# Kernel optimization log

Measured on AMD Instinct MI355X. Metric: run time of the kernel, lower is better.

## Reference

```python
import jax, jax.numpy as jnp
import numpy as np

C = 300      # caption feature dim (word2vec)
OQK = 75     # in_dim // k = 300 // 4 -> query/key channels
H = 128      # adapt_img_hidden (base_proj dim)
LAT = 1024   # image latent size
EPS = 1e-5   # BatchNorm eps


def setup_inputs() -> dict:
    key = jax.random.key(0)
    ks = jax.random.split(key, 16)
    r = lambda i, shape, s=0.05: jax.random.normal(ks[i], shape, dtype=jnp.float32) * s
    return dict(
        img_embed=jax.random.normal(ks[0], (128, 36, LAT), dtype=jnp.float32),
        cap_embed=jax.random.normal(ks[1], (64, 32, C), dtype=jnp.float32),
        # adapt_img: Linear(1024, 128)
        adapt_W=r(2, (H, LAT)), adapt_b=jnp.zeros((H,), jnp.float32),
        # query ProjConv1d: kernel Linear(H, OQK*C), bias Linear(H, OQK), BatchNorm1d(OQK)
        qk_W=r(3, (OQK * C, H)), qk_b=r(4, (OQK * C,)),
        qb_W=r(5, (OQK, H)), qb_b=jnp.zeros((OQK,), jnp.float32),
        q_bn_s=jnp.ones((OQK,), jnp.float32), q_bn_b=jnp.zeros((OQK,), jnp.float32),
        # key ProjConv1d
        kk_W=r(6, (OQK * C, H)), kk_b=r(7, (OQK * C,)),
        kb_W=r(8, (OQK, H)), kb_b=jnp.zeros((OQK,), jnp.float32),
        k_bn_s=jnp.ones((OQK,), jnp.float32), k_bn_b=jnp.zeros((OQK,), jnp.float32),
        # value ProjConv1d: kernel Linear(H, C*C), bias Linear(H, C), BatchNorm1d(C)
        vk_W=r(9, (C * C, H)), vk_b=r(10, (C * C,)),
        vb_W=r(11, (C, H)), vb_b=jnp.zeros((C,), jnp.float32),
        v_bn_s=jnp.ones((C,), jnp.float32), v_bn_b=jnp.zeros((C,), jnp.float32),
        gamma=jnp.float32(0.5),  # residual attention gate (torch inits to 0; 0.5 exercises the path)
        # sim_proj MLP: 300 -> 512 -> 64 -> 1 with BatchNorm+ReLU (dropout = identity at eval)
        W1=r(12, (512, C)), b1=jnp.zeros((512,), jnp.float32),
        bn1_s=jnp.ones((512,), jnp.float32), bn1_b=jnp.zeros((512,), jnp.float32),
        W2=r(13, (64, 512)), b2=jnp.zeros((64,), jnp.float32),
        bn2_s=jnp.ones((64,), jnp.float32), bn2_b=jnp.zeros((64,), jnp.float32),
        W3=r(14, (1, 64)), b3=jnp.zeros((1,), jnp.float32),
    )


def _bn_kernel(kern, s, b):
    # torch: BatchNorm1d(out)(kernel.permute(1,0,2)) with kernel (out, in, ks=1)
    # -> per out-channel stats over the `in` axis (train-mode batch stats)
    mu = kern.mean(axis=1, keepdims=True)
    var = kern.var(axis=1, keepdims=True)
    return (kern - mu) / jnp.sqrt(var + EPS) * s[:, None] + b[:, None]


def _bn_batch(x, s, b):
    # BatchNorm1d over batch axis of (N, C) activations (train-mode stats)
    mu = x.mean(axis=0, keepdims=True)
    var = x.var(axis=0, keepdims=True)
    return (x - mu) / jnp.sqrt(var + EPS) * s + b


def reference(img_embed, cap_embed, adapt_W, adapt_b,
              qk_W, qk_b, qb_W, qb_b, q_bn_s, q_bn_b,
              kk_W, kk_b, kb_W, kb_b, k_bn_s, k_bn_b,
              vk_W, vk_b, vb_W, vb_b, v_bn_s, v_bn_b,
              gamma, W1, b1, bn1_s, bn1_b, W2, b2, bn2_s, bn2_b, W3, b3):
    cap = cap_embed.transpose(0, 2, 1)                      # (Bc, C, T)
    img_mean = img_embed.transpose(0, 2, 1).mean(-1)        # (Bi, LAT): mean over 36 regions
    base = img_mean @ adapt_W.T + adapt_b                   # (Bi, H)

    def per_image(bp):
        # hypernet-generated 1x1 conv kernels, batchnorm-normalized
        Kq = _bn_kernel((qk_W @ bp + qk_b).reshape(OQK, C), q_bn_s, q_bn_b)
        Kk = _bn_kernel((kk_W @ bp + kk_b).reshape(OQK, C), k_bn_s, k_bn_b)
        Kv = _bn_kernel((vk_W @ bp + vk_b).reshape(C, C), v_bn_s, v_bn_b)
        bq = qb_W @ bp + qb_b
        bk = kb_W @ bp + kb_b
        bv = vb_W @ bp + vb_b
        q = jnp.einsum('oc,nct->not', Kq, cap) + bq[:, None]    # (Bc, OQK, T)
        k = jnp.einsum('oc,nct->not', Kk, cap) + bk[:, None]    # (Bc, OQK, T)
        v = jnp.einsum('oc,nct->not', Kv, cap) + bv[:, None]    # (Bc, C, T)
        attn = jax.nn.softmax(jnp.einsum('not,nos->nts', q, k), axis=-1)  # (Bc, T, T)
        sa = jnp.einsum('ncs,nts->nct', v, attn)                # out = V @ attn^T
        x = (gamma * sa + cap).max(-1)                          # (Bc, C): max-pool over tokens
        h = jax.nn.relu(_bn_batch(x @ W1.T + b1, bn1_s, bn1_b))
        h = jax.nn.relu(_bn_batch(h @ W2.T + b2, bn2_s, bn2_b))
        return (h @ W3.T + b3)[:, 0]                            # (Bc,)

    return jax.vmap(per_image)(base)                            # (Bi, Bc)
```

## Files before the change

kernel.cpp:

```cpp
#include <hip/hip_runtime.h>
#include <math.h>

#define EPSB 1e-5f

static const long OFS_BASE  = 0;
static const long OFS_BALL  = 16384;
static const long OFS_MEAN  = 81920;
static const long OFS_CAPB  = 212992;
static const long OFS_RAWP  = 868352;
static const long OFS_X     = 15286272;
static const long OFS_H2    = 17743872;
static const long OFS_H1    = OFS_RAWP;

using bf16x8 = __attribute__((ext_vector_type(8))) __bf16;
using f32x4  = __attribute__((ext_vector_type(4))) float;
#define MFMA16(a, b, c) __builtin_amdgcn_mfma_f32_16x16x32_bf16(a, b, c, 0, 0, 0)

__device__ inline ushort f2bf(float f) {
  const unsigned u = __float_as_uint(f);
  return (ushort)((u + 0x7FFFu + ((u >> 16) & 1u)) >> 16);
}
__device__ inline float bf2f(ushort h) { return __uint_as_float(((unsigned)h) << 16); }

__global__ void k_mean(const float* __restrict__ img, float* __restrict__ mean) {
  const int idx = blockIdx.x * 256 + threadIdx.x;
  const int i = idx >> 10, l = idx & 1023;
  const float* p = img + (size_t)i * 36 * 1024 + l;
  float s = 0.f;
#pragma unroll
  for (int r = 0; r < 36; ++r) s += p[r * 1024];
  mean[idx] = s * (1.0f / 36.0f);
}

__global__ void k_base(const float* __restrict__ mean, const float* __restrict__ W,
                       const float* __restrict__ b, float* __restrict__ base) {
  __shared__ float m_s[1024];
  const int i = blockIdx.x, tid = threadIdx.x;
  for (int k = 0; k < 8; ++k) m_s[tid + 128 * k] = mean[i * 1024 + tid + 128 * k];
  __syncthreads();
  float acc = b[tid];
  const float* wr = W + (size_t)tid * 1024;
#pragma unroll 4
  for (int l = 0; l < 1024; ++l) acc = fmaf(m_s[l], wr[l], acc);
  base[i * 128 + tid] = acc;
}

__global__ void k_bias(const float* __restrict__ qbW, const float* __restrict__ qbb,
                       const float* __restrict__ kbW, const float* __restrict__ kbb,
                       const float* __restrict__ vbW, const float* __restrict__ vbb,
                       const float* __restrict__ base, float* __restrict__ ball) {
  __shared__ float bs[128];
  const int i = blockIdx.y, tid = threadIdx.x;
  if (tid < 128) bs[tid] = base[i * 128 + tid];
  __syncthreads();
  const int o = blockIdx.x * 256 + tid;
  if (o >= 512) return;
  const float* Wr = nullptr;
  float bb = 0.0f;
  if (o < 75)                   { Wr = qbW + (size_t)o * 128;         bb = qbb[o]; }
  else if (o >= 96 && o < 171)  { Wr = kbW + (size_t)(o - 96) * 128;  bb = kbb[o - 96]; }
  else if (o >= 192 && o < 492) { Wr = vbW + (size_t)(o - 192) * 128; bb = vbb[o - 192]; }
  float acc = 0.0f;
  if (Wr) {
#pragma unroll 4
    for (int h = 0; h < 128; ++h) acc = fmaf(Wr[h], bs[h], acc);
    acc += bb;
  }
  ball[i * 512 + o] = acc;
}

__global__ void __launch_bounds__(256) k_capp(const float* __restrict__ cap,
                                              ushort* __restrict__ capP) {
  __shared__ float ct[32 * 301];
  const int n = blockIdx.x, tid = threadIdx.x;
  const float* capn = cap + (size_t)n * 9600;
  {
    const int r = tid >> 3, c8 = tid & 7;
    for (int m = 0; m < 38; ++m) {
      const int c = c8 + 8 * m;
      if (c < 300) ct[r * 301 + c] = capn[r * 300 + c];
    }
  }
  __syncthreads();
  ushort* dst = capP + (size_t)n * 20480;
  for (int u = 0; u < 10; ++u) {
    const int ul = tid + 256 * u;
    const int unit = ul >> 6, lane = ul & 63;
    const int nt = unit / 20, rem = unit % 20;
    const int ks = rem >> 1, pl = rem & 1;
    const int kg = lane >> 4, lr = lane & 15;
    const int t = nt * 16 + lr;
    ushort o8[8];
#pragma unroll
    for (int e = 0; e < 8; ++e) {
      const int c = 32 * ks + 8 * kg + e;
      const float val = (c < 300) ? ct[t * 301 + c] : 0.f;
      const ushort hi = f2bf(val);
      o8[e] = pl ? f2bf(val - bf2f(hi)) : hi;
    }
    uint4 pk;
    pk.x = (uint)o8[0] | ((uint)o8[1] << 16);
    pk.y = (uint)o8[2] | ((uint)o8[3] << 16);
    pk.z = (uint)o8[4] | ((uint)o8[5] << 16);
    pk.w = (uint)o8[6] | ((uint)o8[7] << 16);
    *reinterpret_cast<uint4*>(dst + unit * 512 + lane * 8) = pk;
  }
}

__global__ void __launch_bounds__(256) k_hyp3(
    const float* __restrict__ qkW, const float* __restrict__ qkb,
    const float* __restrict__ kkW, const float* __restrict__ kkb,
    const float* __restrict__ vkW, const float* __restrict__ vkb,
    const float* __restrict__ qs, const float* __restrict__ qb,
    const float* __restrict__ ks_, const float* __restrict__ kb_,
    const float* __restrict__ vs, const float* __restrict__ vb,
    const float* __restrict__ base, ushort* __restrict__ kall) {
  __shared__ float smem[19504];
  __shared__ float scl[64], shf[64];
  const int g = blockIdx.x, half = blockIdx.y, tid = threadIdx.x;
  const int i0g = half * 64;
  const int ot = g >> 4, lr = g & 15;
  const bool isV = (g >= 192);

  const float* Wb = nullptr;
  const float* bvec = nullptr;
  float bns = 0.f, bnb = 0.f;
  if (g < 75)                    { Wb = qkW + (size_t)g * 38400;          bvec = qkb + g * 300;          bns = qs[g];        bnb = qb[g]; }
  else if (g >= 96 && g < 171)   { Wb = kkW + (size_t)(g - 96) * 38400;   bvec = kkb + (g - 96) * 300;   bns = ks_[g - 96];  bnb = kb_[g - 96]; }
  else if (g >= 192 && g < 492)  { Wb = vkW + (size_t)(g - 192) * 38400;  bvec = vkb + (g - 192) * 300;  bns = vs[g - 192];  bnb = vb[g - 192]; }

  if (!Wb) {
    const uint4 z = make_uint4(0, 0, 0, 0);
    if (!isV) {
      for (int m = 0; m < 20; ++m) {
        const int idx = tid + 256 * m;
        const int ii = idx & 63, zz = idx >> 6;
        const int kg2 = zz & 3, pl = (zz >> 2) & 1, ks2 = zz >> 3;
        const size_t off = (size_t)(i0g + ii) * 225280 +
                           (size_t)(ot * 20 + ks2 * 2 + pl) * 512 + (kg2 * 16 + lr) * 8;
        *reinterpret_cast<uint4*>(kall + off) = z;
      }
    } else {
      for (int m = 0; m < 10; ++m) {
        const int idx = tid + 256 * m;
        const int ii = idx & 63, zz = idx >> 6;
        const int kg2 = zz & 3, ks2 = zz >> 2;
        const size_t off = (size_t)(i0g + ii) * 225280 +
                           (size_t)(240 + (ot - 12) * 10 + ks2) * 512 + (kg2 * 16 + lr) * 8;
        *reinterpret_cast<uint4*>(kall + off) = z;
      }
    }
    return;
  }

  for (int m = 0; m < 32; ++m) {
    const int idx = tid + 256 * m;
    const int ii = idx >> 7, h = idx & 127;
    smem[h * 68 + ii] = base[(size_t)(i0g + ii) * 128 + h];
  }

  const int cg = tid >> 2, ig = tid & 3;
  const int c0 = cg * 5, i0 = ig * 16;
  float acc[5][16];
#pragma unroll
  for (int cc = 0; cc < 5; ++cc)
#pragma unroll
    for (int ii = 0; ii < 16; ++ii) acc[cc][ii] = 0.f;
  float* Ws = smem + 8704;
  for (int hc = 0; hc < 4; ++hc) {
    __syncthreads();
    for (int m = 0; m < 10; ++m) {
      const int u = tid + 256 * m;
      if (u < 2400) {
        const int c = u >> 3, h4 = (u & 7) * 4;
        const float4 wv4 = *reinterpret_cast<const float4*>(Wb + (size_t)c * 128 + hc * 32 + h4);
        *reinterpret_cast<float4*>(&Ws[c * 36 + h4]) = wv4;
      }
    }
    __syncthreads();
#pragma unroll 4
    for (int hh = 0; hh < 32; ++hh) {
      const int hg = hc * 32 + hh;
      float bvf[16];
#pragma unroll
      for (int u2 = 0; u2 < 4; ++u2) {
        const float4 b4 = *reinterpret_cast<const float4*>(&smem[hg * 68 + i0 + u2 * 4]);
        bvf[u2 * 4 + 0] = b4.x; bvf[u2 * 4 + 1] = b4.y;
        bvf[u2 * 4 + 2] = b4.z; bvf[u2 * 4 + 3] = b4.w;
      }
#pragma unroll
      for (int cc = 0; cc < 5; ++cc) {
        const float wv = Ws[(c0 + cc) * 36 + hh];
#pragma unroll
        for (int ii = 0; ii < 16; ++ii) acc[cc][ii] = fmaf(wv, bvf[ii], acc[cc][ii]);
      }
    }
  }
  __syncthreads();
#pragma unroll
  for (int cc = 0; cc < 5; ++cc) {
    const int c = c0 + cc;
    if (c < 300) {
      const float bv = bvec[c];
#pragma unroll
      for (int ii = 0; ii < 16; ++ii) smem[c * 64 + i0 + ii] = acc[cc][ii] + bv;
    }
  }
  __syncthreads();
  {
    const int si = tid >> 2, p = tid & 3;
    float s1 = 0.f, s2 = 0.f;
    for (int c = p; c < 300; c += 4) {
      const float x = smem[c * 64 + si];
      s1 += x;
      s2 += x * x;
    }
    s1 += __shfl_xor(s1, 1); s2 += __shfl_xor(s2, 1);
    s1 += __shfl_xor(s1, 2); s2 += __shfl_xor(s2, 2);
    const float mu = s1 * (1.0f / 300.0f);
    const float var = s2 * (1.0f / 300.0f) - mu * mu;
    const float scale = bns / sqrtf(var + EPSB);
    if (p == 0) { scl[si] = scale; shf[si] = bnb - mu * scale; }
  }
  __syncthreads();
  if (!isV) {
    for (int m = 0; m < 20; ++m) {
      const int idx = tid + 256 * m;
      const int ii = idx & 63, zz = idx >> 6;
      const int kg2 = zz & 3, pl = (zz >> 2) & 1, ks2 = zz >> 3;
      const float sc = scl[ii], sh = shf[ii];
      ushort o8[8];
#pragma unroll
      for (int e = 0; e < 8; ++e) {
        const int c = ks2 * 32 + kg2 * 8 + e;
        float val = 0.f;
        if (c < 300) val = fmaf(smem[c * 64 + ii], sc, sh);
        const ushort hi = f2bf(val);
        o8[e] = pl ? f2bf(val - bf2f(hi)) : hi;
      }
      uint4 pk;
      pk.x = (uint)o8[0] | ((uint)o8[1] << 16);
      pk.y = (uint)o8[2] | ((uint)o8[3] << 16);
      pk.z = (uint)o8[4] | ((uint)o8[5] << 16);
      pk.w = (uint)o8[6] | ((uint)o8[7] << 16);
      const size_t off = (size_t)(i0g + ii) * 225280 +
                         (size_t)(ot * 20 + ks2 * 2 + pl) * 512 + (kg2 * 16 + lr) * 8;
      *reinterpret_cast<uint4*>(kall + off) = pk;
    }
  } else {
    for (int m = 0; m < 10; ++m) {
      const int idx = tid + 256 * m;
      const int ii = idx & 63, zz = idx >> 6;
      const int kg2 = zz & 3, ks2 = zz >> 2;
      const float sc = scl[ii], sh = shf[ii];
      ushort o8[8];
#pragma unroll
      for (int e = 0; e < 8; ++e) {
        const int c = ks2 * 32 + kg2 * 8 + e;
        float val = 0.f;
        if (c < 300) val = fmaf(smem[c * 64 + ii], sc, sh);
        o8[e] = f2bf(val);
      }
      uint4 pk;
      pk.x = (uint)o8[0] | ((uint)o8[1] << 16);
      pk.y = (uint)o8[2] | ((uint)o8[3] << 16);
      pk.z = (uint)o8[4] | ((uint)o8[5] << 16);
      pk.w = (uint)o8[6] | ((uint)o8[7] << 16);
      const size_t off = (size_t)(i0g + ii) * 225280 +
                         (size_t)(240 + (ot - 12) * 10 + ks2) * 512 + (kg2 * 16 + lr) * 8;
      *reinterpret_cast<uint4*>(kall + off) = pk;
    }
  }
}

__global__ void __launch_bounds__(256, 4) k_attn10(
    const float* __restrict__ cap, const ushort* __restrict__ kall,
    const ushort* __restrict__ capP, const float* __restrict__ ball,
    const float* __restrict__ gptr, float* __restrict__ x_all) {
  __shared__ ushort qkp[24 * 512];
  __shared__ float sc_s[32 * 36];
  __shared__ ushort at_p[2 * 2 * 64 * 8];
  const int bid = blockIdx.x;
  const int xcd = bid & 7, q = bid >> 3;
  const int i = xcd * 16 + (q >> 6), n = q & 63;
  const int tid = threadIdx.x;
  const int lane = tid & 63, w = tid >> 6;
  const int lrow = lane & 15, kg = lane >> 4;
  const float gamma = gptr[0];
  const ushort* kpL = kall + (size_t)i * 225280 + lane * 8;
  const ushort* cpL = capP + (size_t)n * 20480 + lane * 8;
  const float* bal = ball + i * 512;

  {
    f32x4 acc[3][2];
#pragma unroll
    for (int a = 0; a < 3; ++a)
#pragma unroll
      for (int b2 = 0; b2 < 2; ++b2) acc[a][b2] = (f32x4){0.f, 0.f, 0.f, 0.f};
    bf16x8 AhA[3], AlA[3], AhB[3], AlB[3];
#pragma unroll
    for (int mt = 0; mt < 3; ++mt) {
      const ushort* p = kpL + (size_t)((w * 3 + mt) * 20) * 512;
      AhA[mt] = *reinterpret_cast<const bf16x8*>(p);
      AlA[mt] = *reinterpret_cast<const bf16x8*>(p + 512);
    }
#pragma unroll
    for (int kp = 0; kp < 5; ++kp) {
      {
        const int ks = 2 * kp;
        bf16x8 Bh[2], Bl[2];
#pragma unroll
        for (int nt = 0; nt < 2; ++nt) {
          const ushort* p = cpL + (size_t)(nt * 20 + ks * 2) * 512;
          Bh[nt] = *reinterpret_cast<const bf16x8*>(p);
          Bl[nt] = *reinterpret_cast<const bf16x8*>(p + 512);
        }
#pragma unroll
        for (int mt = 0; mt < 3; ++mt) {
          const ushort* p = kpL + (size_t)((w * 3 + mt) * 20 + (ks + 1) * 2) * 512;
          AhB[mt] = *reinterpret_cast<const bf16x8*>(p);
          AlB[mt] = *reinterpret_cast<const bf16x8*>(p + 512);
        }
#pragma unroll
        for (int mt = 0; mt < 3; ++mt)
#pragma unroll
          for (int nt = 0; nt < 2; ++nt) {
            acc[mt][nt] = MFMA16(AhA[mt], Bh[nt], acc[mt][nt]);
            acc[mt][nt] = MFMA16(AhA[mt], Bl[nt], acc[mt][nt]);
            acc[mt][nt] = MFMA16(AlA[mt], Bh[nt], acc[mt][nt]);
          }
      }
      {
        const int ks = 2 * kp + 1;
        bf16x8 Bh[2], Bl[2];
#pragma unroll
        for (int nt = 0; nt < 2; ++nt) {
          const ushort* p = cpL + (size_t)(nt * 20 + ks * 2) * 512;
          Bh[nt] = *reinterpret_cast<const bf16x8*>(p);
          Bl[nt] = *reinterpret_cast<const bf16x8*>(p + 512);
        }
        if (kp < 4) {
#pragma unroll
          for (int mt = 0; mt < 3; ++mt) {
            const ushort* p = kpL + (size_t)((w * 3 + mt) * 20 + (ks + 1) * 2) * 512;
            AhA[mt] = *reinterpret_cast<const bf16x8*>(p);
            AlA[mt] = *reinterpret_cast<const bf16x8*>(p + 512);
          }
        }
#pragma unroll
        for (int mt = 0; mt < 3; ++mt)
#pragma unroll
          for (int nt = 0; nt < 2; ++nt) {
            acc[mt][nt] = MFMA16(AhB[mt], Bh[nt], acc[mt][nt]);
            acc[mt][nt] = MFMA16(AhB[mt], Bl[nt], acc[mt][nt]);
            acc[mt][nt] = MFMA16(AlB[mt], Bh[nt], acc[mt][nt]);
          }
      }
    }
#pragma unroll
    for (int mt = 0; mt < 3; ++mt)
#pragma unroll
      for (int nt = 0; nt < 2; ++nt)
#pragma unroll
        for (int r = 0; r < 4; ++r) {
          const int og = w * 48 + mt * 16 + kg * 4 + r;
          const float val = acc[mt][nt][r] + bal[og];
          const ushort hi = f2bf(val);
          const ushort lo = f2bf(val - bf2f(hi));
          const int os = (w < 2) ? og : og - 96;
          const int ub = ((w < 2) ? 0 : 12) + nt * 6 + (os >> 5) * 2;
          const int lp = ((os & 31) >> 3) * 16 + lrow;
          const int e = os & 7;
          qkp[(ub + 0) * 512 + lp * 8 + e] = hi;
          qkp[(ub + 1) * 512 + lp * 8 + e] = lo;
        }
  }
  __syncthreads();

  {
    const int tt = w >> 1, st = w & 1;
    bf16x8 Aq[3][2], Bk[3][2];
#pragma unroll
    for (int k3 = 0; k3 < 3; ++k3)
#pragma unroll
      for (int pl = 0; pl < 2; ++pl) {
        Aq[k3][pl] = *reinterpret_cast<const bf16x8*>(&qkp[(tt * 6 + k3 * 2 + pl) * 512 + lane * 8]);
        Bk[k3][pl] = *reinterpret_cast<const bf16x8*>(&qkp[(12 + st * 6 + k3 * 2 + pl) * 512 + lane * 8]);
      }
    f32x4 D = (f32x4){0.f, 0.f, 0.f, 0.f};
#pragma unroll
    for (int k3 = 0; k3 < 3; ++k3) {
      D = MFMA16(Aq[k3][0], Bk[k3][0], D);
      D = MFMA16(Aq[k3][0], Bk[k3][1], D);
      D = MFMA16(Aq[k3][1], Bk[k3][0], D);
      D = MFMA16(Aq[k3][1], Bk[k3][1], D);
    }
#pragma unroll
    for (int r = 0; r < 4; ++r)
      sc_s[(tt * 16 + kg * 4 + r) * 36 + st * 16 + lrow] = D[r];
  }
  __syncthreads();

  {
    const int sg = tid & 7, tq = tid >> 3;
    const int s0 = sg * 4;
    const float4 sv = *reinterpret_cast<const float4*>(&sc_s[tq * 36 + s0]);
    float sc[4] = {sv.x, sv.y, sv.z, sv.w};
    float m = fmaxf(fmaxf(sc[0], sc[1]), fmaxf(sc[2], sc[3]));
    m = fmaxf(m, __shfl_xor(m, 1));
    m = fmaxf(m, __shfl_xor(m, 2));
    m = fmaxf(m, __shfl_xor(m, 4));
    float ev[4], ssum = 0.f;
#pragma unroll
    for (int u = 0; u < 4; ++u) { ev[u] = expf(sc[u] - m); ssum += ev[u]; }
    ssum += __shfl_xor(ssum, 1);
    ssum += __shfl_xor(ssum, 2);
    ssum += __shfl_xor(ssum, 4);
    const float inv = 1.0f / ssum;
    const int tt = tq >> 4, lrp = tq & 15, kgp = sg >> 1, eb = (sg & 1) * 4;
    ushort h4[4], l4[4];
#pragma unroll
    for (int u = 0; u < 4; ++u) {
      const float val = ev[u] * inv;
      const ushort hi = f2bf(val);
      h4[u] = hi;
      l4[u] = f2bf(val - bf2f(hi));
    }
    uint2 ph, pl2;
    ph.x = (uint)h4[0] | ((uint)h4[1] << 16);
    ph.y = (uint)h4[2] | ((uint)h4[3] << 16);
    pl2.x = (uint)l4[0] | ((uint)l4[1] << 16);
    pl2.y = (uint)l4[2] | ((uint)l4[3] << 16);
    *reinterpret_cast<uint2*>(&at_p[((tt * 2 + 0) * 64 + kgp * 16 + lrp) * 8 + eb]) = ph;
    *reinterpret_cast<uint2*>(&at_p[((tt * 2 + 1) * 64 + kgp * 16 + lrp) * 8 + eb]) = pl2;
  }
  __syncthreads();

  ushort* vt = qkp;
#pragma unroll
  for (int ch = 0; ch < 2; ++ch) {
    const int TB = 12 + ch * 12;
    const int RB = TB * 16;
    const int nmt = ch ? 2 : 3;
    f32x4 vacc[3][2];
#pragma unroll
    for (int a = 0; a < 3; ++a)
#pragma unroll
      for (int b2 = 0; b2 < 2; ++b2) vacc[a][b2] = (f32x4){0.f, 0.f, 0.f, 0.f};
    bf16x8 AvA[3], AvB[3];
    for (int mi = 0; mi < nmt; ++mi)
      AvA[mi] = *reinterpret_cast<const bf16x8*>(
          kpL + (size_t)(240 + (TB - 12 + w + mi * 4) * 10) * 512);
#pragma unroll
    for (int kp = 0; kp < 5; ++kp) {
      {
        const int ks = 2 * kp;
        bf16x8 Bh[2];
#pragma unroll
        for (int nt = 0; nt < 2; ++nt)
          Bh[nt] = *reinterpret_cast<const bf16x8*>(cpL + (size_t)(nt * 20 + ks * 2) * 512);
        for (int mi = 0; mi < nmt; ++mi)
          AvB[mi] = *reinterpret_cast<const bf16x8*>(
              kpL + (size_t)(240 + (TB - 12 + w + mi * 4) * 10 + ks + 1) * 512);
        for (int mi = 0; mi < nmt; ++mi)
#pragma unroll
          for (int nt = 0; nt < 2; ++nt)
            vacc[mi][nt] = MFMA16(AvA[mi], Bh[nt], vacc[mi][nt]);
      }
      {
        const int ks = 2 * kp + 1;
        bf16x8 Bh[2];
#pragma unroll
        for (int nt = 0; nt < 2; ++nt)
          Bh[nt] = *reinterpret_cast<const bf16x8*>(cpL + (size_t)(nt * 20 + ks * 2) * 512);
        if (kp < 4) {
          for (int mi = 0; mi < nmt; ++mi)
            AvA[mi] = *reinterpret_cast<const bf16x8*>(
                kpL + (size_t)(240 + (TB - 12 + w + mi * 4) * 10 + ks + 1) * 512);
        }
        for (int mi = 0; mi < nmt; ++mi)
#pragma unroll
          for (int nt = 0; nt < 2; ++nt)
            vacc[mi][nt] = MFMA16(AvB[mi], Bh[nt], vacc[mi][nt]);
      }
    }
    if (ch) __syncthreads();
    for (int mi = 0; mi < nmt; ++mi) {
      const int tile = w + mi * 4;
#pragma unroll
      for (int nt = 0; nt < 2; ++nt) {
        const int kgp = nt * 2 + (lrow >> 3), ee = lrow & 7;
#pragma unroll
        for (int r = 0; r < 4; ++r) {
          const int vl = tile * 16 + kg * 4 + r;
          const float val = vacc[mi][nt][r] + bal[RB + vl];
          const ushort hi = f2bf(val);
          vt[((tile * 2 + 0) * 64 + kgp * 16 + kg * 4 + r) * 8 + ee] = hi;
          vt[((tile * 2 + 1) * 64 + kgp * 16 + kg * 4 + r) * 8 + ee] = f2bf(val - bf2f(hi));
        }
      }
    }
    __syncthreads();
    {
      bf16x8 ah[2], al[2];
#pragma unroll
      for (int tt = 0; tt < 2; ++tt) {
        ah[tt] = *reinterpret_cast<const bf16x8*>(&at_p[((tt * 2 + 0) * 64 + lane) * 8]);
        al[tt] = *reinterpret_cast<const bf16x8*>(&at_p[((tt * 2 + 1) * 64 + lane) * 8]);
      }
      const int npw = ch ? 2 : 3;
      for (int j = 0; j < npw; ++j) {
        const int ct = w * npw + j;
        const int c0 = ch * 192 + ct * 16 + (lane >> 4) * 4;
        const bf16x8 vh  = *reinterpret_cast<const bf16x8*>(&vt[((ct * 2 + 0) * 64 + lane) * 8]);
        const bf16x8 vl8 = *reinterpret_cast<const bf16x8*>(&vt[((ct * 2 + 1) * 64 + lane) * 8]);
        f32x4 a0 = (f32x4){0.f, 0.f, 0.f, 0.f}, a1 = (f32x4){0.f, 0.f, 0.f, 0.f};
        a0 = MFMA16(vh, ah[0], a0);
        a0 = MFMA16(vh, al[0], a0);
        a0 = MFMA16(vl8, ah[0], a0);
        a1 = MFMA16(vh, ah[1], a1);
        a1 = MFMA16(vh, al[1], a1);
        a1 = MFMA16(vl8, ah[1], a1);
        if (c0 < 300) {
          const int t0 = lane & 15;
          const float4 c4a = *reinterpret_cast<const float4*>(&cap[(size_t)n * 9600 + t0 * 300 + c0]);
          const float4 c4b = *reinterpret_cast<const float4*>(&cap[(size_t)n * 9600 + (t0 + 16) * 300 + c0]);
          float mx[4];
          mx[0] = fmaxf(fmaf(gamma, a0[0], c4a.x), fmaf(gamma, a1[0], c4b.x));
          mx[1] = fmaxf(fmaf(gamma, a0[1], c4a.y), fmaf(gamma, a1[1], c4b.y));
          mx[2] = fmaxf(fmaf(gamma, a0[2], c4a.z), fmaf(gamma, a1[2], c4b.z));
          mx[3] = fmaxf(fmaf(gamma, a0[3], c4a.w), fmaf(gamma, a1[3], c4b.w));
#pragma unroll
          for (int mmask = 1; mmask < 16; mmask <<= 1)
#pragma unroll
            for (int r = 0; r < 4; ++r) mx[r] = fmaxf(mx[r], __shfl_xor(mx[r], mmask));
          if ((lane & 15) == 0)
            *reinterpret_cast<float4*>(&x_all[((size_t)i * 64 + n) * 300 + c0]) =
                make_float4(mx[0], mx[1], mx[2], mx[3]);
        }
      }
    }
  }
}

__global__ void __launch_bounds__(256, 4) k_h1b(
    const float* __restrict__ x_all, const float* __restrict__ W1,
    const float* __restrict__ b1, const float* __restrict__ bn1s,
    const float* __restrict__ bn1b, float* __restrict__ h1) {
  __shared__ float xt[32 * 68];
  __shared__ float wt[32 * 132];
  __shared__ float sc1[128], sh1[128];
  const int ec = blockIdx.x, i = blockIdx.y, tid = threadIdx.x;
  const int e0c = ec * 128;
  const int eg = tid & 15, ng = tid >> 4;
  const int e0 = eg * 8, n0 = ng * 4;
  float acc[4][8] = {};
  for (int cb = 0; cb < 10; ++cb) {
    const int c0 = cb * 32;
    __syncthreads();
    for (int k = 0; k < 8; ++k) {
      const int idx = tid + 256 * k;
      const int nn = idx >> 5, cl = idx & 31;
      const int c = c0 + cl;
      xt[cl * 68 + nn] = (c < 300) ? x_all[((size_t)i * 64 + nn) * 300 + c] : 0.0f;
    }
    for (int k = 0; k < 16; ++k) {
      const int idx = tid + 256 * k;
      const int ee = idx >> 5, cl = idx & 31;
      const int c = c0 + cl;
      wt[cl * 132 + ee] = (c < 300) ? W1[(size_t)(e0c + ee) * 300 + c] : 0.0f;
    }
    __syncthreads();
#pragma unroll 4
    for (int cl = 0; cl < 32; ++cl) {
      const float4 xv = *reinterpret_cast<const float4*>(&xt[cl * 68 + n0]);
      const float4 wa = *reinterpret_cast<const float4*>(&wt[cl * 132 + e0]);
      const float4 wb = *reinterpret_cast<const float4*>(&wt[cl * 132 + e0 + 4]);
      const float xv4[4] = {xv.x, xv.y, xv.z, xv.w};
      const float wv8[8] = {wa.x, wa.y, wa.z, wa.w, wb.x, wb.y, wb.z, wb.w};
#pragma unroll
      for (int u = 0; u < 4; ++u)
#pragma unroll
        for (int v = 0; v < 8; ++v) acc[u][v] = fmaf(xv4[u], wv8[v], acc[u][v]);
    }
  }
  float b1v[8];
#pragma unroll
  for (int v = 0; v < 8; ++v) b1v[v] = b1[e0c + e0 + v];
  float val[4][8];
#pragma unroll
  for (int u = 0; u < 4; ++u)
#pragma unroll
    for (int v = 0; v < 8; ++v) val[u][v] = acc[u][v] + b1v[v];
  __syncthreads();
  float* ps1 = xt;
  float* ps2 = wt;
#pragma unroll
  for (int v = 0; v < 8; ++v) {
    float su = 0.f, sq = 0.f;
#pragma unroll
    for (int u = 0; u < 4; ++u) { su += val[u][v]; sq += val[u][v] * val[u][v]; }
    ps1[ng * 132 + e0 + v] = su;
    ps2[ng * 132 + e0 + v] = sq;
  }
  __syncthreads();
  if (tid < 128) {
    const int e = tid;
    float s1 = 0.f, s2 = 0.f;
#pragma unroll 4
    for (int gq = 0; gq < 16; ++gq) { s1 += ps1[gq * 132 + e]; s2 += ps2[gq * 132 + e]; }
    const float mu = s1 * (1.0f / 64.0f);
    const float var = s2 * (1.0f / 64.0f) - mu * mu;
    const float scale = bn1s[e0c + e] / sqrtf(var + EPSB);
    sc1[e] = scale;
    sh1[e] = bn1b[e0c + e] - mu * scale;
  }
  __syncthreads();
#pragma unroll
  for (int u = 0; u < 4; ++u) {
    float o8[8];
#pragma unroll
    for (int v = 0; v < 8; ++v)
      o8[v] = fmaxf(fmaf(val[u][v], sc1[e0 + v], sh1[e0 + v]), 0.0f);
    float* dst = h1 + ((size_t)i * 64 + n0 + u) * 512 + e0c + e0;
    *reinterpret_cast<float4*>(dst) = make_float4(o8[0], o8[1], o8[2], o8[3]);
    *reinterpret_cast<float4*>(dst + 4) = make_float4(o8[4], o8[5], o8[6], o8[7]);
  }
}

__global__ void __launch_bounds__(256) k_h2(
    const float* __restrict__ h1, const float* __restrict__ W2,
    const float* __restrict__ b2, float* __restrict__ h2buf) {
  __shared__ float h1s[32 * 517];
  const int jn = blockIdx.x, i = blockIdx.y, tid = threadIdx.x;
  const int bn = jn * 32;
  for (int m = 0; m < 64; ++m) {
    const int idx = tid + 256 * m;
    h1s[(idx >> 9) * 517 + (idx & 511)] = h1[((size_t)i * 64 + bn) * 512 + idx];
  }
  __syncthreads();
  const int dg = tid & 15, ng2 = tid >> 4;
  const int d0 = dg * 4, n0 = ng2 * 2;
  float a0[4] = {}, a1[4] = {};
#pragma unroll 4
  for (int e = 0; e < 512; ++e) {
    const float h0 = h1s[n0 * 517 + e];
    const float h1v = h1s[(n0 + 1) * 517 + e];
#pragma unroll
    for (int v = 0; v < 4; ++v) {
      const float wv = W2[(size_t)(d0 + v) * 512 + e];
      a0[v] = fmaf(h0, wv, a0[v]);
      a1[v] = fmaf(h1v, wv, a1[v]);
    }
  }
  const float4 bb = *reinterpret_cast<const float4*>(&b2[d0]);
  float* dst0 = h2buf + ((size_t)i * 64 + bn + n0) * 64 + d0;
  *reinterpret_cast<float4*>(dst0) = make_float4(a0[0] + bb.x, a0[1] + bb.y, a0[2] + bb.z, a0[3] + bb.w);
  *reinterpret_cast<float4*>(dst0 + 64) = make_float4(a1[0] + bb.x, a1[1] + bb.y, a1[2] + bb.z, a1[3] + bb.w);
}

__global__ void __launch_bounds__(256) k_out(
    const float* __restrict__ h2buf, const float* __restrict__ bn2s,
    const float* __restrict__ bn2b, const float* __restrict__ W3,
    const float* __restrict__ b3, float* __restrict__ out) {
  __shared__ float h2s[64 * 65];
  const int i = blockIdx.x, tid = threadIdx.x;
  for (int m = 0; m < 16; ++m) {
    const int idx = tid + 256 * m;
    h2s[(idx >> 6) * 65 + (idx & 63)] = h2buf[(size_t)i * 4096 + idx];
  }
  __syncthreads();
  if (tid < 64) {
    const int d = tid;
    float s1 = 0.f, s2 = 0.f;
    for (int nn = 0; nn < 64; ++nn) {
      const float v = h2s[nn * 65 + d];
      s1 += v;
      s2 += v * v;
    }
    const float mu = s1 * (1.0f / 64.0f);
    const float var = s2 * (1.0f / 64.0f) - mu * mu;
    const float scale = bn2s[d] / sqrtf(var + EPSB);
    const float shift = bn2b[d] - mu * scale;
    for (int nn = 0; nn < 64; ++nn)
      h2s[nn * 65 + d] = fmaxf(fmaf(h2s[nn * 65 + d], scale, shift), 0.0f);
  }
  __syncthreads();
  if (tid < 64) {
    const int nn = tid;
    float acc = b3[0];
    for (int d = 0; d < 64; ++d) acc = fmaf(h2s[nn * 65 + d], W3[d], acc);
    out[i * 64 + nn] = acc;
  }
}

extern "C" void kernel_launch(void* const* d_in, const int* in_sizes, int n_in,
                              void* d_out, int out_size, void* d_ws, size_t ws_size,
                              hipStream_t stream) {
  const float* img  = (const float*)d_in[0];
  const float* cap  = (const float*)d_in[1];
  const float* adW  = (const float*)d_in[2];
  const float* adb  = (const float*)d_in[3];
  const float* qkW  = (const float*)d_in[4];
  const float* qkb  = (const float*)d_in[5];
  const float* qbW  = (const float*)d_in[6];
  const float* qbb  = (const float*)d_in[7];
  const float* qbns = (const float*)d_in[8];
  const float* qbnb = (const float*)d_in[9];
  const float* kkW  = (const float*)d_in[10];
  const float* kkb  = (const float*)d_in[11];
  const float* kbW  = (const float*)d_in[12];
  const float* kbb  = (const float*)d_in[13];
  const float* kbns = (const float*)d_in[14];
  const float* kbnb = (const float*)d_in[15];
  const float* vkW  = (const float*)d_in[16];
  const float* vkb  = (const float*)d_in[17];
  const float* vbW  = (const float*)d_in[18];
  const float* vbb  = (const float*)d_in[19];
  const float* vbns = (const float*)d_in[20];
  const float* vbnb = (const float*)d_in[21];
  const float* gamma= (const float*)d_in[22];
  const float* W1   = (const float*)d_in[23];
  const float* b1   = (const float*)d_in[24];
  const float* bn1s = (const float*)d_in[25];
  const float* bn1b = (const float*)d_in[26];
  const float* W2   = (const float*)d_in[27];
  const float* b2   = (const float*)d_in[28];
  const float* bn2s = (const float*)d_in[29];
  const float* bn2b = (const float*)d_in[30];
  const float* W3   = (const float*)d_in[31];
  const float* b3   = (const float*)d_in[32];

  float* ws    = (float*)d_ws;
  float* base  = ws + OFS_BASE;
  float* ball  = ws + OFS_BALL;
  float* mean  = ws + OFS_MEAN;
  ushort* capP = (ushort*)(ws + OFS_CAPB);
  ushort* kall = (ushort*)(ws + OFS_RAWP);
  float* x_all = ws + OFS_X;
  float* h2buf = ws + OFS_H2;
  float* h1    = ws + OFS_H1;
  float* out   = (float*)d_out;

  k_mean<<<512, 256, 0, stream>>>(img, mean);
  k_base<<<128, 128, 0, stream>>>(mean, adW, adb, base);
  k_bias<<<dim3(2, 128), 256, 0, stream>>>(qbW, qbb, kbW, kbb, vbW, vbb, base, ball);
  k_capp<<<64, 256, 0, stream>>>(cap, capP);
  k_hyp3<<<dim3(512, 2), 256, 0, stream>>>(qkW, qkb, kkW, kkb, vkW, vkb,
                                           qbns, qbnb, kbns, kbnb, vbns, vbnb, base, kall);
  k_attn10<<<8192, 256, 0, stream>>>(cap, kall, capP, ball, gamma, x_all);
  k_h1b<<<dim3(4, 128), 256, 0, stream>>>(x_all, W1, b1, bn1s, bn1b, h1);
  k_h2<<<dim3(2, 128), 256, 0, stream>>>(h1, W2, b2, h2buf);
  k_out<<<128, 256, 0, stream>>>(h2buf, bn2s, bn2b, W3, b3, out);
}
```

Before: 550.4 us.

## Move hypernet kernel generation to split-bf16 MFMA and skip padded tiles

The hypernetwork GEMM that builds per-image conv kernels moves from scalar FP32 FMA to bf16 MFMA with hi/lo splitting, so it keeps roughly FP32 accuracy. A new small kernel pre-packs the base projections into MFMA B-operand layout. Padding blocks in the hypernet grid now exit early. The attention kernel skips the third M-tile on odd waves, which covers only padded Q/K rows. This adds LDS transposition and conversion work and a small extra launch, and the three-term split drops the lo*lo product, which carries some precision risk.

```diff
diff --git a/kernel.cpp b/kernel.cpp
--- a/kernel.cpp
+++ b/kernel.cpp
@@ -10,6 +10,7 @@
 static const long OFS_RAWP  = 868352;
 static const long OFS_X     = 15286272;
 static const long OFS_H2    = 17743872;
+static const long OFS_BASP  = 18268160;
 static const long OFS_H1    = OFS_RAWP;
 
 using bf16x8 = __attribute__((ext_vector_type(8))) __bf16;
@@ -43,6 +44,31 @@
 #pragma unroll 4
   for (int l = 0; l < 1024; ++l) acc = fmaf(m_s[l], wr[l], acc);
   base[i * 128 + tid] = acc;
+}
+
+__global__ void __launch_bounds__(256) k_basp(const float* __restrict__ base,
+                                              ushort* __restrict__ basP) {
+  const int half = blockIdx.x, tid = threadIdx.x;
+  for (int m = 0; m < 8; ++m) {
+    const int u = tid + 256 * m;
+    const int ln = u & 63, unit = u >> 6;
+    const int it = unit >> 3, ks = (unit >> 1) & 3, pl = unit & 1;
+    const int i = half * 64 + it * 16 + (ln & 15);
+    const int h = ks * 32 + (ln >> 4) * 8;
+    ushort o8[8];
+#pragma unroll
+    for (int e = 0; e < 8; ++e) {
+      const float v = base[(size_t)i * 128 + h + e];
+      const ushort hi = f2bf(v);
+      o8[e] = pl ? f2bf(v - bf2f(hi)) : hi;
+    }
+    uint4 pk;
+    pk.x = (uint)o8[0] | ((uint)o8[1] << 16);
+    pk.y = (uint)o8[2] | ((uint)o8[3] << 16);
+    pk.z = (uint)o8[4] | ((uint)o8[5] << 16);
+    pk.w = (uint)o8[6] | ((uint)o8[7] << 16);
+    *reinterpret_cast<uint4*>(basP + (size_t)(half * 32 + unit) * 512 + ln * 8) = pk;
+  }
 }
 
 __global__ void k_bias(const float* __restrict__ qbW, const float* __restrict__ qbb,
@@ -107,20 +133,21 @@
   }
 }
 
-__global__ void __launch_bounds__(256) k_hyp3(
+__global__ void __launch_bounds__(256) k_hyp4(
     const float* __restrict__ qkW, const float* __restrict__ qkb,
     const float* __restrict__ kkW, const float* __restrict__ kkb,
     const float* __restrict__ vkW, const float* __restrict__ vkb,
     const float* __restrict__ qs, const float* __restrict__ qb,
     const float* __restrict__ ks_, const float* __restrict__ kb_,
     const float* __restrict__ vs, const float* __restrict__ vb,
-    const float* __restrict__ base, ushort* __restrict__ kall) {
-  __shared__ float smem[19504];
+    const ushort* __restrict__ basP, ushort* __restrict__ kall) {
+  __shared__ float smem[19760];
   __shared__ float scl[64], shf[64];
   const int g = blockIdx.x, half = blockIdx.y, tid = threadIdx.x;
   const int i0g = half * 64;
   const int ot = g >> 4, lr = g & 15;
   const bool isV = (g >= 192);
+  if ((g >= 80 && g < 96) || (g >= 176 && g < 192)) return;
 
   const float* Wb = nullptr;
   const float* bvec = nullptr;
@@ -153,65 +180,84 @@
     return;
   }
 
-  for (int m = 0; m < 32; ++m) {
-    const int idx = tid + 256 * m;
-    const int ii = idx >> 7, h = idx & 127;
-    smem[h * 68 + ii] = base[(size_t)(i0g + ii) * 128 + h];
-  }
-
-  const int cg = tid >> 2, ig = tid & 3;
-  const int c0 = cg * 5, i0 = ig * 16;
-  float acc[5][16];
-#pragma unroll
-  for (int cc = 0; cc < 5; ++cc)
-#pragma unroll
-    for (int ii = 0; ii < 16; ++ii) acc[cc][ii] = 0.f;
-  float* Ws = smem + 8704;
+  const int lane = tid & 63, w = tid >> 6;
+  const int lrow = lane & 15, kg = lane >> 4;
+  ushort* Af = reinterpret_cast<ushort*>(smem + 9760);
+
+  f32x4 acc[19];
+#pragma unroll
+  for (int ct = 0; ct < 19; ++ct) acc[ct] = (f32x4){0.f, 0.f, 0.f, 0.f};
+
   for (int hc = 0; hc < 4; ++hc) {
     __syncthreads();
     for (int m = 0; m < 10; ++m) {
       const int u = tid + 256 * m;
-      if (u < 2400) {
+      if (u < 2432) {
         const int c = u >> 3, h4 = (u & 7) * 4;
-        const float4 wv4 = *reinterpret_cast<const float4*>(Wb + (size_t)c * 128 + hc * 32 + h4);
-        *reinterpret_cast<float4*>(&Ws[c * 36 + h4]) = wv4;
+        float4 wv = make_float4(0.f, 0.f, 0.f, 0.f);
+        if (c < 300) wv = *reinterpret_cast<const float4*>(Wb + (size_t)c * 128 + hc * 32 + h4);
+        smem[(h4 + 0) * 305 + c] = wv.x;
+        smem[(h4 + 1) * 305 + c] = wv.y;
+        smem[(h4 + 2) * 305 + c] = wv.z;
+        smem[(h4 + 3) * 305 + c] = wv.w;
       }
     }
     __syncthreads();
-#pragma unroll 4
-    for (int hh = 0; hh < 32; ++hh) {
-      const int hg = hc * 32 + hh;
-      float bvf[16];
-#pragma unroll
-      for (int u2 = 0; u2 < 4; ++u2) {
-        const float4 b4 = *reinterpret_cast<const float4*>(&smem[hg * 68 + i0 + u2 * 4]);
-        bvf[u2 * 4 + 0] = b4.x; bvf[u2 * 4 + 1] = b4.y;
-        bvf[u2 * 4 + 2] = b4.z; bvf[u2 * 4 + 3] = b4.w;
-      }
-#pragma unroll
-      for (int cc = 0; cc < 5; ++cc) {
-        const float wv = Ws[(c0 + cc) * 36 + hh];
-#pragma unroll
-        for (int ii = 0; ii < 16; ++ii) acc[cc][ii] = fmaf(wv, bvf[ii], acc[cc][ii]);
-      }
-    }
-  }
-  __syncthreads();
-#pragma unroll
-  for (int cc = 0; cc < 5; ++cc) {
-    const int c = c0 + cc;
-    if (c < 300) {
-      const float bv = bvec[c];
-#pragma unroll
-      for (int ii = 0; ii < 16; ++ii) smem[c * 64 + i0 + ii] = acc[cc][ii] + bv;
-    }
-  }
+    for (int m = 0; m < 5; ++m) {
+      const int u = tid + 256 * m;
+      if (u < 1216) {
+        const int ln = u & 63, ct = u >> 6;
+        const int cc = ct * 16 + (ln & 15);
+        const int hb = (ln >> 4) * 8;
+        ushort h8[8], l8[8];
+#pragma unroll
+        for (int e = 0; e < 8; ++e) {
+          const float v = smem[(hb + e) * 305 + cc];
+          const ushort hi = f2bf(v);
+          h8[e] = hi;
+          l8[e] = f2bf(v - bf2f(hi));
+        }
+        uint4 ph, pl4;
+        ph.x = (uint)h8[0] | ((uint)h8[1] << 16);
+        ph.y = (uint)h8[2] | ((uint)h8[3] << 16);
+        ph.z = (uint)h8[4] | ((uint)h8[5] << 16);
+        ph.w = (uint)h8[6] | ((uint)h8[7] << 16);
+        pl4.x = (uint)l8[0] | ((uint)l8[1] << 16);
+        pl4.y = (uint)l8[2] | ((uint)l8[3] << 16);
+        pl4.z = (uint)l8[4] | ((uint)l8[5] << 16);
+        pl4.w = (uint)l8[6] | ((uint)l8[7] << 16);
+        *reinterpret_cast<uint4*>(&Af[(ct * 2 + 0) * 512 + ln * 8]) = ph;
+        *reinterpret_cast<uint4*>(&Af[(ct * 2 + 1) * 512 + ln * 8]) = pl4;
+      }
+    }
+    const bf16x8 Bh = *reinterpret_cast<const bf16x8*>(
+        basP + (size_t)(half * 32 + w * 8 + hc * 2 + 0) * 512 + lane * 8);
+    const bf16x8 Bl = *reinterpret_cast<const bf16x8*>(
+        basP + (size_t)(half * 32 + w * 8 + hc * 2 + 1) * 512 + lane * 8);
+    __syncthreads();
+#pragma unroll
+    for (int ct = 0; ct < 19; ++ct) {
+      const bf16x8 Ah = *reinterpret_cast<const bf16x8*>(&Af[(ct * 2 + 0) * 512 + lane * 8]);
+      const bf16x8 Al = *reinterpret_cast<const bf16x8*>(&Af[(ct * 2 + 1) * 512 + lane * 8]);
+      acc[ct] = MFMA16(Ah, Bh, acc[ct]);
+      acc[ct] = MFMA16(Ah, Bl, acc[ct]);
+      acc[ct] = MFMA16(Al, Bh, acc[ct]);
+    }
+  }
+  __syncthreads();
+#pragma unroll
+  for (int ct = 0; ct < 19; ++ct)
+#pragma unroll
+    for (int r = 0; r < 4; ++r) {
+      const int c = ct * 16 + kg * 4 + r;
+      if (c < 300) smem[c * 65 + w * 16 + lrow] = acc[ct][r] + bvec[c];
+    }
   __syncthreads();
   {
     const int si = tid >> 2, p = tid & 3;
     float s1 = 0.f, s2 = 0.f;
     for (int c = p; c < 300; c += 4) {
-      const float x = smem[c * 64 + si];
+      const float x = smem[c * 65 + si];
       s1 += x;
       s2 += x * x;
     }
@@ -234,7 +280,7 @@
       for (int e = 0; e < 8; ++e) {
         const int c = ks2 * 32 + kg2 * 8 + e;
         float val = 0.f;
-        if (c < 300) val = fmaf(smem[c * 64 + ii], sc, sh);
+        if (c < 300) val = fmaf(smem[c * 65 + ii], sc, sh);
         const ushort hi = f2bf(val);
         o8[e] = pl ? f2bf(val - bf2f(hi)) : hi;
       }
@@ -258,7 +304,7 @@
       for (int e = 0; e < 8; ++e) {
         const int c = ks2 * 32 + kg2 * 8 + e;
         float val = 0.f;
-        if (c < 300) val = fmaf(smem[c * 64 + ii], sc, sh);
+        if (c < 300) val = fmaf(smem[c * 65 + ii], sc, sh);
         o8[e] = f2bf(val);
       }
       uint4 pk;
@@ -273,7 +319,7 @@
   }
 }
 
-__global__ void __launch_bounds__(256, 4) k_attn10(
+__global__ void __launch_bounds__(256, 4) k_attn11(
     const float* __restrict__ cap, const ushort* __restrict__ kall,
     const ushort* __restrict__ capP, const float* __restrict__ ball,
     const float* __restrict__ gptr, float* __restrict__ x_all) {
@@ -290,6 +336,7 @@
   const ushort* kpL = kall + (size_t)i * 225280 + lane * 8;
   const ushort* cpL = capP + (size_t)n * 20480 + lane * 8;
   const float* bal = ball + i * 512;
+  const bool oddw = (w & 1);
 
   {
     f32x4 acc[3][2];
@@ -299,11 +346,12 @@
       for (int b2 = 0; b2 < 2; ++b2) acc[a][b2] = (f32x4){0.f, 0.f, 0.f, 0.f};
     bf16x8 AhA[3], AlA[3], AhB[3], AlB[3];
 #pragma unroll
-    for (int mt = 0; mt < 3; ++mt) {
-      const ushort* p = kpL + (size_t)((w * 3 + mt) * 20) * 512;
-      AhA[mt] = *reinterpret_cast<const bf16x8*>(p);
-      AlA[mt] = *reinterpret_cast<const bf16x8*>(p + 512);
-    }
+    for (int mt = 0; mt < 3; ++mt)
+      if (!oddw || mt < 2) {
+        const ushort* p = kpL + (size_t)((w * 3 + mt) * 20) * 512;
+        AhA[mt] = *reinterpret_cast<const bf16x8*>(p);
+        AlA[mt] = *reinterpret_cast<const bf16x8*>(p + 512);
+      }
 #pragma unroll
     for (int kp = 0; kp < 5; ++kp) {
       {
@@ -316,19 +364,21 @@
           Bl[nt] = *reinterpret_cast<const bf16x8*>(p + 512);
         }
 #pragma unroll
-        for (int mt = 0; mt < 3; ++mt) {
-          const ushort* p = kpL + (size_t)((w * 3 + mt) * 20 + (ks + 1) * 2) * 512;
-          AhB[mt] = *reinterpret_cast<const bf16x8*>(p);
-          AlB[mt] = *reinterpret_cast<const bf16x8*>(p + 512);
-        }
-#pragma unroll
         for (int mt = 0; mt < 3; ++mt)
-#pragma unroll
-          for (int nt = 0; nt < 2; ++nt) {
-            acc[mt][nt] = MFMA16(AhA[mt], Bh[nt], acc[mt][nt]);
-            acc[mt][nt] = MFMA16(AhA[mt], Bl[nt], acc[mt][nt]);
-            acc[mt][nt] = MFMA16(AlA[mt], Bh[nt], acc[mt][nt]);
+          if (!oddw || mt < 2) {
+            const ushort* p = kpL + (size_t)((w * 3 + mt) * 20 + (ks + 1) * 2) * 512;
+            AhB[mt] = *reinterpret_cast<const bf16x8*>(p);
+            AlB[mt] = *reinterpret_cast<const bf16x8*>(p + 512);
           }
+#pragma unroll
+        for (int mt = 0; mt < 3; ++mt)
+          if (!oddw || mt < 2)
+#pragma unroll
+            for (int nt = 0; nt < 2; ++nt) {
+              acc[mt][nt] = MFMA16(AhA[mt], Bh[nt], acc[mt][nt]);
+              acc[mt][nt] = MFMA16(AhA[mt], Bl[nt], acc[mt][nt]);
+              acc[mt][nt] = MFMA16(AlA[mt], Bh[nt], acc[mt][nt]);
+            }
       }
       {
         const int ks = 2 * kp + 1;
@@ -341,20 +391,22 @@
         }
         if (kp < 4) {
 #pragma unroll
-          for (int mt = 0; mt < 3; ++mt) {
-            const ushort* p = kpL + (size_t)((w * 3 + mt) * 20 + (ks + 1) * 2) * 512;
-            AhA[mt] = *reinterpret_cast<const bf16x8*>(p);
-            AlA[mt] = *reinterpret_cast<const bf16x8*>(p + 512);
-          }
+          for (int mt = 0; mt < 3; ++mt)
+            if (!oddw || mt < 2) {
+              const ushort* p = kpL + (size_t)((w * 3 + mt) * 20 + (ks + 1) * 2) * 512;
+              AhA[mt] = *reinterpret_cast<const bf16x8*>(p);
+              AlA[mt] = *reinterpret_cast<const bf16x8*>(p + 512);
+            }
         }
 #pragma unroll
         for (int mt = 0; mt < 3; ++mt)
-#pragma unroll
-          for (int nt = 0; nt < 2; ++nt) {
-            acc[mt][nt] = MFMA16(AhB[mt], Bh[nt], acc[mt][nt]);
-            acc[mt][nt] = MFMA16(AhB[mt], Bl[nt], acc[mt][nt]);
-            acc[mt][nt] = MFMA16(AlB[mt], Bh[nt], acc[mt][nt]);
-          }
+          if (!oddw || mt < 2)
+#pragma unroll
+            for (int nt = 0; nt < 2; ++nt) {
+              acc[mt][nt] = MFMA16(AhB[mt], Bh[nt], acc[mt][nt]);
+              acc[mt][nt] = MFMA16(AhB[mt], Bl[nt], acc[mt][nt]);
+              acc[mt][nt] = MFMA16(AlB[mt], Bh[nt], acc[mt][nt]);
+            }
       }
     }
 #pragma unroll
@@ -739,16 +791,18 @@
   ushort* kall = (ushort*)(ws + OFS_RAWP);
   float* x_all = ws + OFS_X;
   float* h2buf = ws + OFS_H2;
+  ushort* basP = (ushort*)(ws + OFS_BASP);
   float* h1    = ws + OFS_H1;
   float* out   = (float*)d_out;
 
   k_mean<<<512, 256, 0, stream>>>(img, mean);
   k_base<<<128, 128, 0, stream>>>(mean, adW, adb, base);
+  k_basp<<<2, 256, 0, stream>>>(base, basP);
   k_bias<<<dim3(2, 128), 256, 0, stream>>>(qbW, qbb, kbW, kbb, vbW, vbb, base, ball);
   k_capp<<<64, 256, 0, stream>>>(cap, capP);
-  k_hyp3<<<dim3(512, 2), 256, 0, stream>>>(qkW, qkb, kkW, kkb, vkW, vkb,
-                                           qbns, qbnb, kbns, kbnb, vbns, vbnb, base, kall);
-  k_attn10<<<8192, 256, 0, stream>>>(cap, kall, capP, ball, gamma, x_all);
+  k_hyp4<<<dim3(512, 2), 256, 0, stream>>>(qkW, qkb, kkW, kkb, vkW, vkb,
+                                           qbns, qbnb, kbns, kbnb, vbns, vbnb, basP, kall);
+  k_attn11<<<8192, 256, 0, stream>>>(cap, kall, capP, ball, gamma, x_all);
   k_h1b<<<dim3(4, 128), 256, 0, stream>>>(x_all, W1, b1, bn1s, bn1b, h1);
   k_h2<<<dim3(2, 128), 256, 0, stream>>>(h1, W2, b2, h2buf);
   k_out<<<128, 256, 0, stream>>>(h2buf, bn2s, bn2b, W3, b3, out);
```

New measurement: 516.4 us. -6.2%, faster.
